# Kernel tuning notes

Hardware: AMD Instinct MI355X
Metric: run time of the kernel (lower is better)

## Reference

```python
import jax, jax.numpy as jnp
import numpy as np

EPS = 1e-5

def _graph_conv(x, src, dst, W, b, N):
    # DGL GraphConv, norm='both': D_out^{-1/2} then aggregate then D_in^{-1/2}
    ones = jnp.ones((src.shape[0],), x.dtype)
    out_deg = jnp.clip(jax.ops.segment_sum(ones, src, num_segments=N), 1.0)
    in_deg = jnp.clip(jax.ops.segment_sum(ones, dst, num_segments=N), 1.0)
    h = (x * (out_deg ** -0.5)[:, None]) @ W          # [N, out] (mult W before gather)
    agg = jax.ops.segment_sum(h[src], dst, num_segments=N)  # [N, out] irregular scatter
    return agg * (in_deg ** -0.5)[:, None] + b

def _bn_relu(h, gamma, beta):
    # BatchNorm1d in training mode: batch stats over node axis (biased var)
    mu = jnp.mean(h, axis=0)
    var = jnp.mean((h - mu) ** 2, axis=0)
    return jax.nn.relu((h - mu) * jax.lax.rsqrt(var + EPS) * gamma + beta)

def setup_inputs() -> dict:
    key = jax.random.key(0)
    ks = jax.random.split(key, 6)
    N, E, F, H, C = 100000, 1000000, 128, 128, 16
    return {
        "x": jax.random.normal(ks[0], (N, F), dtype=jnp.float32),
        "src": jax.random.randint(ks[1], (E,), 0, N, dtype=jnp.int32),
        "dst": jax.random.randint(ks[2], (E,), 0, N, dtype=jnp.int32),
        "W1": jax.random.normal(ks[3], (F, H), dtype=jnp.float32) * 0.05,
        "b1": jnp.zeros((H,), jnp.float32),
        "g1": jnp.ones((H,), jnp.float32),
        "be1": jnp.zeros((H,), jnp.float32),
        "W2": jax.random.normal(ks[4], (H, H), dtype=jnp.float32) * 0.05,
        "b2": jnp.zeros((H,), jnp.float32),
        "g2": jnp.ones((H,), jnp.float32),
        "be2": jnp.zeros((H,), jnp.float32),
        "Wc": jax.random.normal(ks[5], (H, C), dtype=jnp.float32) * 0.05,
        "bc": jnp.zeros((C,), jnp.float32),
    }

def reference(x, src, dst, W1, b1, g1, be1, W2, b2, g2, be2, Wc, bc):
    N = x.shape[0]
    h = _bn_relu(_graph_conv(x, src, dst, W1, b1, N), g1, be1)  # dropout = identity (eval)
    h = _bn_relu(_graph_conv(h, src, dst, W2, b2, N), g2, be2)
    return h @ Wc + bc  # [N, num_cls]
```

## Files before the change

### kernel.cpp

```cpp
#include <hip/hip_runtime.h>

#define FDIM 128
#define MAXDEG 64
#define GATHERB 2048
#define NREP 32

#define RSIZE 128
#define RSHIFT 7
#define RCAP 1024
#define CCAP 14336
#define PCAP 80

typedef unsigned short ushort_t;
typedef unsigned int uint_t;
typedef __attribute__((ext_vector_type(8))) short short8;
typedef __attribute__((ext_vector_type(16))) float float16;

__device__ __forceinline__ float bflo(uint_t u) { return __uint_as_float(u << 16); }
__device__ __forceinline__ float bfhi(uint_t u) { return __uint_as_float(u & 0xffff0000u); }
__device__ __forceinline__ ushort_t f2bf(float f) {
    uint_t u = __float_as_uint(f);
    return (ushort_t)((u + 0x7fffu + ((u >> 16) & 1u)) >> 16);
}
__device__ __forceinline__ uint_t pack2bf(float lo, float hi) {
    return (uint_t)f2bf(lo) | ((uint_t)f2bf(hi) << 16);
}

__global__ __launch_bounds__(256) void gemm1_kernel(
    const float* __restrict__ x, const float* __restrict__ W,
    ushort_t* __restrict__ outb, int N) {
    int idx = blockIdx.x;
    int t = threadIdx.x;
    __shared__ float xt[16][FDIM];
    int base = idx * 16;
    const float4* x4 = (const float4*)x;
#pragma unroll
    for (int i = 0; i < 2; i++) {
        int ii = t + i * 256;
        int row = ii >> 5, c4 = ii & 31;
        int grow = base + row;
        float4 v = make_float4(0.f, 0.f, 0.f, 0.f);
        if (grow < N) v = x4[(size_t)grow * 32 + c4];
        *(float4*)&xt[row][c4 * 4] = v;
    }
    __syncthreads();
    int rg = t >> 6, c = t & 63;
    float acc[4][2] = {};
    const float* Wc0 = W + c;
    for (int k4 = 0; k4 < 32; k4++) {
        float xv[16];
#pragma unroll
        for (int r = 0; r < 4; r++) {
            float4 tmp = *(const float4*)&xt[rg * 4 + r][k4 * 4];
            xv[r * 4 + 0] = tmp.x; xv[r * 4 + 1] = tmp.y;
            xv[r * 4 + 2] = tmp.z; xv[r * 4 + 3] = tmp.w;
        }
#pragma unroll
        for (int kk = 0; kk < 4; kk++) {
            float w0 = Wc0[(k4 * 4 + kk) * FDIM];
            float w1 = Wc0[(k4 * 4 + kk) * FDIM + 64];
#pragma unroll
            for (int r = 0; r < 4; r++) {
                acc[r][0] = fmaf(xv[r * 4 + kk], w0, acc[r][0]);
                acc[r][1] = fmaf(xv[r * 4 + kk], w1, acc[r][1]);
            }
        }
    }
#pragma unroll
    for (int r = 0; r < 4; r++) {
        int grow = base + rg * 4 + r;
        if (grow < N) {
            outb[(size_t)grow * FDIM + c] = f2bf(acc[r][0]);
            outb[(size_t)grow * FDIM + c + 64] = f2bf(acc[r][1]);
        }
    }
}

__global__ __launch_bounds__(256) void bucket_kernel(
    const int* __restrict__ src, const int* __restrict__ dst,
    uint_t* __restrict__ bktD, int* __restrict__ baseD,
    uint_t* __restrict__ bktS, int* __restrict__ baseS,
    int E, int P, int R) {
    __shared__ uint4 buf4[CCAP / 4];
    __shared__ int hist[RCAP];
    __shared__ int scanbuf[256];
    uint_t* buf = (uint_t*)buf4;
    int t = threadIdx.x;
    int role = blockIdx.x >= P;
    int p = role ? blockIdx.x - P : blockIdx.x;
    const int* key = role ? src : dst;
    int e0 = p * CCAP;
    int e1 = min(E, e0 + CCAP);
    int cnt = e1 - e0;

    for (int r = t; r < R; r += 256) hist[r] = 0;
    __syncthreads();
    for (int i = e0 + t; i < e1; i += 256) atomicAdd(&hist[key[i] >> RSHIFT], 1);
    __syncthreads();

    int b0 = t * 4;
    int hv[4];
    int s0 = 0;
#pragma unroll
    for (int k = 0; k < 4; k++) {
        hv[k] = (b0 + k < R) ? hist[b0 + k] : 0;
        s0 += hv[k];
    }
    scanbuf[t] = s0;
    __syncthreads();
    for (int off = 1; off < 256; off <<= 1) {
        int v = (t >= off) ? scanbuf[t - off] : 0;
        __syncthreads();
        scanbuf[t] += v;
        __syncthreads();
    }
    int run = scanbuf[t] - s0;
    int* baseG = role ? baseS : baseD;
#pragma unroll
    for (int k = 0; k < 4; k++) {
        if (b0 + k < R) {
            baseG[(b0 + k) * P + p] = run;
            hist[b0 + k] = run;
        }
        run += hv[k];
    }
    if (t == 0) baseG[R * P + p] = cnt;
    __syncthreads();

    for (int i = e0 + t; i < e1; i += 256) {
        int kv = key[i];
        int slot = atomicAdd(&hist[kv >> RSHIFT], 1);
        uint_t entry = role ? (uint_t)kv
                            : (((uint_t)(kv & (RSIZE - 1)) << 25) | (uint_t)src[i]);
        buf[slot] = entry;
    }
    __syncthreads();

    uint_t* outp = role ? bktS : bktD;
    uint4* og = (uint4*)(outp + (size_t)e0);
    int n4 = (cnt + 3) >> 2;
    for (int j = t; j < n4; j += 256) og[j] = buf4[j];
}

__global__ __launch_bounds__(256) void build_kernel(
    const uint_t* __restrict__ bktD, const int* __restrict__ baseD,
    const uint_t* __restrict__ bktS, const int* __restrict__ baseS,
    int* __restrict__ eidx, int* __restrict__ cnt, int* __restrict__ cs,
    int N, int P) {
    __shared__ uint4 ell4[RSIZE][MAXDEG / 4];
    __shared__ int cntN[RSIZE], csN[RSIZE];
    __shared__ int dB0[PCAP], dB1[PCAP], sB0[PCAP], sB1[PCAP];
    uint_t* ell = (uint_t*)ell4;
    int t = threadIdx.x;
    int r = blockIdx.x;

    if (t < RSIZE) { cntN[t] = 0; csN[t] = 0; }
    for (int i = t; i < P; i += 256) {
        dB0[i] = baseD[r * P + i];
        dB1[i] = baseD[(r + 1) * P + i];
        sB0[i] = baseS[r * P + i];
        sB1[i] = baseS[(r + 1) * P + i];
    }
    __syncthreads();

    int wave = t >> 6, lane = t & 63;
    for (int p = wave; p < P; p += 4) {
        int b = dB0[p], len = dB1[p] - b;
        const uint_t* seg = bktD + (size_t)p * CCAP + b;
        for (int i = lane; i < len; i += 64) {
            uint_t e = seg[i];
            int dl = e >> 25;
            uint_t s = e & 0x1FFFFFFu;
            int slot = atomicAdd(&cntN[dl], 1);
            if (slot < MAXDEG) ell[dl * MAXDEG + slot] = s;
        }
        int b2 = sB0[p], len2 = sB1[p] - b2;
        const uint_t* seg2 = bktS + (size_t)p * CCAP + b2;
        for (int i = lane; i < len2; i += 64)
            atomicAdd(&csN[seg2[i] & (RSIZE - 1)], 1);
    }
    __syncthreads();

    int base = r * RSIZE;
    for (int i = t; i < RSIZE * (MAXDEG / 4); i += 256) {
        int n = i >> 4, q = i & 15;
        int g = base + n;
        if (g < N && q * 4 < min(cntN[n], MAXDEG))
            ((uint4*)eidx)[(size_t)g * (MAXDEG / 4) + q] = ell4[n][q];
    }
    if (t < RSIZE) {
        int g = base + t;
        if (g < N) { cnt[g] = cntN[t]; cs[g] = csN[t]; }
    }
}

template <bool OS>
__global__ __launch_bounds__(256) void gather_kernel(const ushort_t* __restrict__ hb,
                                                     const int* __restrict__ eidx,
                                                     const int* __restrict__ cnt,
                                                     const int* __restrict__ cs,
                                                     const float* __restrict__ b,
                                                     ushort_t* __restrict__ outb,
                                                     float* __restrict__ statsRep, int N) {
    __shared__ float4 redS[256];
    __shared__ float4 redQ[256];
    int t = threadIdx.x;
    int wave = t >> 6, lane = t & 63;
    int half = lane >> 5, sub = lane & 31;
    int gw = blockIdx.x * 4 + wave;
    const uint2* h2 = (const uint2*)hb;
    uint2* o2 = (uint2*)outb;
    float4 bb = ((const float4*)b)[sub];
    float st0 = 0, st1 = 0, st2 = 0, st3 = 0, sq0 = 0, sq1 = 0, sq2 = 0, sq3 = 0;

    for (int node = gw; node < N; node += GATHERB * 4) {
        int deg = cnt[node];
        int e = min(deg, MAXDEG);
        const int* row = eidx + (size_t)node * MAXDEG;
        int ridx = (lane < e) ? row[lane] : 0;
        float scv = 1.f;
        if (OS) scv = (lane < e) ? rsqrtf((float)max(cs[ridx], 1)) : 0.f;

        float a0 = 0, a1 = 0, a2 = 0, a3 = 0;
        float c0 = 0, c1 = 0, c2 = 0, c3 = 0;
        int j = 0;
        for (; j + 3 < e; j += 4) {
            int iA = __shfl(ridx, j + half);
            int iB = __shfl(ridx, j + 2 + half);
            float sA = OS ? __shfl(scv, j + half) : 1.f;
            float sB = OS ? __shfl(scv, j + 2 + half) : 1.f;
            uint2 uA = h2[(size_t)iA * 32 + sub];
            uint2 uB = h2[(size_t)iB * 32 + sub];
            a0 = fmaf(bflo(uA.x), sA, a0); a1 = fmaf(bfhi(uA.x), sA, a1);
            a2 = fmaf(bflo(uA.y), sA, a2); a3 = fmaf(bfhi(uA.y), sA, a3);
            c0 = fmaf(bflo(uB.x), sB, c0); c1 = fmaf(bfhi(uB.x), sB, c1);
            c2 = fmaf(bflo(uB.y), sB, c2); c3 = fmaf(bfhi(uB.y), sB, c3);
        }
        for (; j < e; j += 2) {
            int jj = j + half;
            bool take = jj < e;
            int i0 = __shfl(ridx, take ? jj : (e - 1));
            float s0 = take ? (OS ? __shfl(scv, jj) : 1.f) : 0.f;
            uint2 u = h2[(size_t)i0 * 32 + sub];
            a0 = fmaf(bflo(u.x), s0, a0); a1 = fmaf(bfhi(u.x), s0, a1);
            a2 = fmaf(bflo(u.y), s0, a2); a3 = fmaf(bfhi(u.y), s0, a3);
        }
        a0 += c0; a1 += c1; a2 += c2; a3 += c3;
        a0 += __shfl_xor(a0, 32);
        a1 += __shfl_xor(a1, 32);
        a2 += __shfl_xor(a2, 32);
        a3 += __shfl_xor(a3, 32);
        if (half == 0) {
            float isc = rsqrtf((float)max(deg, 1));
            uint2 o;
            o.x = pack2bf(fmaf(a0, isc, bb.x), fmaf(a1, isc, bb.y));
            o.y = pack2bf(fmaf(a2, isc, bb.z), fmaf(a3, isc, bb.w));
            o2[(size_t)node * 32 + sub] = o;
            float v0 = bflo(o.x), v1 = bfhi(o.x), v2 = bflo(o.y), v3 = bfhi(o.y);
            st0 += v0; st1 += v1; st2 += v2; st3 += v3;
            sq0 = fmaf(v0, v0, sq0); sq1 = fmaf(v1, v1, sq1);
            sq2 = fmaf(v2, v2, sq2); sq3 = fmaf(v3, v3, sq3);
        }
    }

    redS[t] = make_float4(st0, st1, st2, st3);
    redQ[t] = make_float4(sq0, sq1, sq2, sq3);
    __syncthreads();
    if (t < 32) {
        float4 s = make_float4(0, 0, 0, 0), q = make_float4(0, 0, 0, 0);
#pragma unroll
        for (int w = 0; w < 4; w++) {
            float4 a = redS[w * 64 + t];
            float4 z = redQ[w * 64 + t];
            s.x += a.x; s.y += a.y; s.z += a.z; s.w += a.w;
            q.x += z.x; q.y += z.y; q.z += z.z; q.w += z.w;
        }
        float* dstp = statsRep + (size_t)(blockIdx.x & (NREP - 1)) * 256;
        atomicAdd(&dstp[t * 4 + 0], s.x);
        atomicAdd(&dstp[t * 4 + 1], s.y);
        atomicAdd(&dstp[t * 4 + 2], s.z);
        atomicAdd(&dstp[t * 4 + 3], s.w);
        atomicAdd(&dstp[128 + t * 4 + 0], q.x);
        atomicAdd(&dstp[128 + t * 4 + 1], q.y);
        atomicAdd(&dstp[128 + t * 4 + 2], q.z);
        atomicAdd(&dstp[128 + t * 4 + 3], q.w);
    }
}

__global__ __launch_bounds__(256) void gemm2_kernel(const ushort_t* __restrict__ hb,
                                                    const float* __restrict__ W,
                                                    const int* __restrict__ cs,
                                                    const float* __restrict__ statsRep,
                                                    const float* __restrict__ g,
                                                    const float* __restrict__ be,
                                                    ushort_t* __restrict__ outb, int N,
                                                    float invN) {
    __shared__ ushort_t zt[64][136];
    __shared__ ushort_t wt[128][136];
    __shared__ float Ash[FDIM], Bsh[FDIM];
    int t = threadIdx.x;
    int base = blockIdx.x * 64;

    if (t < FDIM) {
        float s = 0.f, q = 0.f;
        for (int r = 0; r < NREP; r++) {
            s += statsRep[r * 256 + t];
            q += statsRep[r * 256 + 128 + t];
        }
        float mu = s * invN;
        float var = q * invN - mu * mu;
        float a = g[t] * rsqrtf(var + 1e-5f);
        Ash[t] = a;
        Bsh[t] = be[t] - mu * a;
    }
    for (int i = t; i < FDIM * FDIM; i += 256) {
        int k = i >> 7, n = i & 127;
        wt[n][k] = f2bf(W[i]);
    }
    __syncthreads();

    const uint_t* h1 = (const uint_t*)hb;
    for (int i = t; i < 64 * 64; i += 256) {
        int row = i >> 6, cp = i & 63;
        int grow = base + row;
        uint_t o = 0;
        if (grow < N) {
            uint_t u = h1[(size_t)grow * 64 + cp];
            float s = rsqrtf((float)max(cs[grow], 1));
            float v0 = fmaxf(fmaf(bflo(u), Ash[cp * 2], Bsh[cp * 2]), 0.f) * s;
            float v1 = fmaxf(fmaf(bfhi(u), Ash[cp * 2 + 1], Bsh[cp * 2 + 1]), 0.f) * s;
            o = pack2bf(v0, v1);
        }
        *(uint_t*)&zt[row][cp * 2] = o;
    }
    __syncthreads();

    int wv = t >> 6, lane = t & 63;
    int rt = wv >> 1;
    int m = lane & 31;
    int kg = lane >> 5;

    short8 af[8];
#pragma unroll
    for (int kk = 0; kk < 8; kk++)
        af[kk] = *(const short8*)&zt[rt * 32 + m][kk * 16 + kg * 8];

#pragma unroll
    for (int cc = 0; cc < 2; cc++) {
        int ct = (wv & 1) * 2 + cc;
        float16 acc = {0, 0, 0, 0, 0, 0, 0, 0, 0, 0, 0, 0, 0, 0, 0, 0};
#pragma unroll
        for (int kk = 0; kk < 8; kk++) {
            short8 bf = *(const short8*)&wt[ct * 32 + m][kk * 16 + kg * 8];
            acc = __builtin_amdgcn_mfma_f32_32x32x16_bf16(af[kk], bf, acc, 0, 0, 0);
        }
        int col = ct * 32 + m;
#pragma unroll
        for (int r = 0; r < 16; r++) {
            int row = base + rt * 32 + (r & 3) + 8 * (r >> 2) + 4 * kg;
            if (row < N) outb[(size_t)row * FDIM + col] = f2bf(acc[r]);
        }
    }
}

__global__ __launch_bounds__(256) void cls_kernel(const ushort_t* __restrict__ hb,
                                                  const float* __restrict__ Wc,
                                                  const float* __restrict__ bc,
                                                  const float* __restrict__ statsRep,
                                                  const float* __restrict__ g,
                                                  const float* __restrict__ be,
                                                  float* __restrict__ out, int N, float invN) {
    __shared__ float wcl[FDIM * 16];
    __shared__ float red[16][256];
    __shared__ float Ash[FDIM], Bsh[FDIM];
    int t = threadIdx.x;
    int base = blockIdx.x * 64;
#pragma unroll
    for (int i = 0; i < 8; i++) wcl[t + i * 256] = Wc[t + i * 256];
    if (t < FDIM) {
        float s = 0.f, q = 0.f;
        for (int r = 0; r < NREP; r++) {
            s += statsRep[r * 256 + t];
            q += statsRep[r * 256 + 128 + t];
        }
        float mu = s * invN;
        float var = q * invN - mu * mu;
        float a = g[t] * rsqrtf(var + 1e-5f);
        Ash[t] = a;
        Bsh[t] = be[t] - mu * a;
    }
    __syncthreads();

    int node = base + (t >> 2);
    int q4 = t & 3;
    float acc[16];
#pragma unroll
    for (int c = 0; c < 16; c++) acc[c] = 0.f;

    if (node < N) {
        const uint2* hu2 = (const uint2*)((const uint_t*)hb + (size_t)node * 64 + q4 * 16);
        const float* Af = Ash + q4 * 32;
        const float* Bf = Bsh + q4 * 32;
#pragma unroll 1
        for (int kk = 0; kk < 8; kk++) {
            uint2 u = hu2[kk];
            float4 ab = *(const float4*)&Af[kk * 4];
            float4 bb = *(const float4*)&Bf[kk * 4];
            float v0 = fmaxf(fmaf(bflo(u.x), ab.x, bb.x), 0.f);
            float v1 = fmaxf(fmaf(bfhi(u.x), ab.y, bb.y), 0.f);
            float v2 = fmaxf(fmaf(bflo(u.y), ab.z, bb.z), 0.f);
            float v3 = fmaxf(fmaf(bfhi(u.y), ab.w, bb.w), 0.f);
            int k0 = q4 * 32 + kk * 4;
            const float* w0 = &wcl[k0 * 16];
#pragma unroll
            for (int c = 0; c < 16; c++) {
                float s = fmaf(v0, w0[c], fmaf(v1, w0[16 + c], fmaf(v2, w0[32 + c], v3 * w0[48 + c])));
                acc[c] += s;
            }
        }
    }
#pragma unroll
    for (int c = 0; c < 16; c++) red[c][t] = acc[c];
    __syncthreads();
#pragma unroll
    for (int i = t; i < 64 * 16; i += 256) {
        int n = i >> 4, c = i & 15;
        float4 p = *(const float4*)&red[c][n * 4];
        int grow = base + n;
        if (grow < N) out[(size_t)grow * 16 + c] = (p.x + p.y) + (p.z + p.w) + bc[c];
    }
}

extern "C" void kernel_launch(void* const* d_in, const int* in_sizes, int n_in,
                              void* d_out, int out_size, void* d_ws, size_t ws_size,
                              hipStream_t stream) {
    const float* x  = (const float*)d_in[0];
    const int* src  = (const int*)d_in[1];
    const int* dst  = (const int*)d_in[2];
    const float* W1 = (const float*)d_in[3];
    const float* b1 = (const float*)d_in[4];
    const float* g1 = (const float*)d_in[5];
    const float* be1= (const float*)d_in[6];
    const float* W2 = (const float*)d_in[7];
    const float* b2 = (const float*)d_in[8];
    const float* g2 = (const float*)d_in[9];
    const float* be2= (const float*)d_in[10];
    const float* Wc = (const float*)d_in[11];
    const float* bc = (const float*)d_in[12];
    float* out = (float*)d_out;

    int N = in_sizes[0] / FDIM;
    int E = in_sizes[1];
    size_t NB = (size_t)N * FDIM;

    ushort_t* bufA = (ushort_t*)d_ws;
    ushort_t* bufB = bufA + NB;
    int* cs        = (int*)(bufB + NB);
    int* cnt       = cs + N;
    float* statsR1 = (float*)(cnt + N);
    float* statsR2 = statsR1 + NREP * 256;
    int* eidx      = (int*)(statsR2 + NREP * 256);

    uint_t* bktD = (uint_t*)bufB;
    uint_t* bktS = bktD + (size_t)PCAP * CCAP;
    int* baseD   = (int*)(bktS + (size_t)PCAP * CCAP);
    int* baseS   = baseD + (RCAP + 1) * PCAP;

    int P = (E + CCAP - 1) / CCAP;
    int R = (N + RSIZE - 1) >> RSHIFT;

    hipMemsetAsync(statsR1, 0, (size_t)2 * NREP * 256 * sizeof(float), stream);

    bucket_kernel<<<2 * P, 256, 0, stream>>>(src, dst, bktD, baseD, bktS, baseS, E, P, R);
    build_kernel<<<R, 256, 0, stream>>>(bktD, baseD, bktS, baseS, eidx, cnt, cs, N, P);

    int gemmB = (N + 15) / 16;
    gemm1_kernel<<<gemmB, 256, 0, stream>>>(x, W1, bufA, N);

    float invN = 1.0f / N;

    gather_kernel<true><<<GATHERB, 256, 0, stream>>>(bufA, eidx, cnt, cs, b1, bufB, statsR1, N);

    gemm2_kernel<<<(N + 63) / 64, 256, 0, stream>>>(bufB, W2, cs, statsR1, g1, be1, bufA, N, invN);
    gather_kernel<false><<<GATHERB, 256, 0, stream>>>(bufA, eidx, cnt, nullptr, b2, bufB, statsR2, N);

    cls_kernel<<<(N + 63) / 64, 256, 0, stream>>>(bufB, Wc, bc, statsR2, g2, be2, out, N, invN);
}
```

Baseline: 390.1 us.

## Use bf16 MFMA for first GEMM and pre-convert weights once in bucket kernel

The scalar fp32 FMA gemm1 is replaced by a 64-row-tile kernel that converts x to bf16 in shared memory and computes with 32x32x16 bf16 MFMA instructions. Both weight matrices are now transposed and converted to bf16 once by extra blocks appended to the bucket kernel, so gemm1 and gemm2 load pre-packed bf16 weights with vector loads instead of converting per block. Rounding x to bf16 before the multiply lowers input precision for the first layer.

```diff
diff --git a/kernel.cpp b/kernel.cpp
--- a/kernel.cpp
+++ b/kernel.cpp
@@ -10,6 +10,7 @@
 #define RCAP 1024
 #define CCAP 14336
 #define PCAP 80
+#define WCONVB 8
 
 typedef unsigned short ushort_t;
 typedef unsigned int uint_t;
@@ -27,51 +28,56 @@
 }
 
 __global__ __launch_bounds__(256) void gemm1_kernel(
-    const float* __restrict__ x, const float* __restrict__ W,
+    const float* __restrict__ x, const ushort_t* __restrict__ wb,
     ushort_t* __restrict__ outb, int N) {
-    int idx = blockIdx.x;
+    __shared__ ushort_t zt[64][136];
+    __shared__ ushort_t wt[128][136];
     int t = threadIdx.x;
-    __shared__ float xt[16][FDIM];
-    int base = idx * 16;
+    int base = blockIdx.x * 64;
+
+    const uint4* wb4 = (const uint4*)wb;
+    for (int i = t; i < FDIM * 16; i += 256) {
+        int n = i >> 4, q = i & 15;
+        *(uint4*)&wt[n][q * 8] = wb4[n * 16 + q];
+    }
     const float4* x4 = (const float4*)x;
-#pragma unroll
-    for (int i = 0; i < 2; i++) {
-        int ii = t + i * 256;
-        int row = ii >> 5, c4 = ii & 31;
+    for (int i = t; i < 64 * 32; i += 256) {
+        int row = i >> 5, c4 = i & 31;
         int grow = base + row;
-        float4 v = make_float4(0.f, 0.f, 0.f, 0.f);
-        if (grow < N) v = x4[(size_t)grow * 32 + c4];
-        *(float4*)&xt[row][c4 * 4] = v;
-    }
-    __syncthreads();
-    int rg = t >> 6, c = t & 63;
-    float acc[4][2] = {};
-    const float* Wc0 = W + c;
-    for (int k4 = 0; k4 < 32; k4++) {
-        float xv[16];
-#pragma unroll
-        for (int r = 0; r < 4; r++) {
-            float4 tmp = *(const float4*)&xt[rg * 4 + r][k4 * 4];
-            xv[r * 4 + 0] = tmp.x; xv[r * 4 + 1] = tmp.y;
-            xv[r * 4 + 2] = tmp.z; xv[r * 4 + 3] = tmp.w;
-        }
-#pragma unroll
-        for (int kk = 0; kk < 4; kk++) {
-            float w0 = Wc0[(k4 * 4 + kk) * FDIM];
-            float w1 = Wc0[(k4 * 4 + kk) * FDIM + 64];
-#pragma unroll
-            for (int r = 0; r < 4; r++) {
-                acc[r][0] = fmaf(xv[r * 4 + kk], w0, acc[r][0]);
-                acc[r][1] = fmaf(xv[r * 4 + kk], w1, acc[r][1]);
-            }
-        }
-    }
-#pragma unroll
-    for (int r = 0; r < 4; r++) {
-        int grow = base + rg * 4 + r;
+        uint2 o = make_uint2(0u, 0u);
         if (grow < N) {
-            outb[(size_t)grow * FDIM + c] = f2bf(acc[r][0]);
-            outb[(size_t)grow * FDIM + c + 64] = f2bf(acc[r][1]);
+            float4 v = x4[(size_t)grow * 32 + c4];
+            o.x = pack2bf(v.x, v.y);
+            o.y = pack2bf(v.z, v.w);
+        }
+        *(uint2*)&zt[row][c4 * 4] = o;
+    }
+    __syncthreads();
+
+    int wv = t >> 6, lane = t & 63;
+    int rt = wv >> 1;
+    int m = lane & 31;
+    int kg = lane >> 5;
+
+    short8 af[8];
+#pragma unroll
+    for (int kk = 0; kk < 8; kk++)
+        af[kk] = *(const short8*)&zt[rt * 32 + m][kk * 16 + kg * 8];
+
+#pragma unroll
+    for (int cc = 0; cc < 2; cc++) {
+        int ct = (wv & 1) * 2 + cc;
+        float16 acc = {0, 0, 0, 0, 0, 0, 0, 0, 0, 0, 0, 0, 0, 0, 0, 0};
+#pragma unroll
+        for (int kk = 0; kk < 8; kk++) {
+            short8 bf = *(const short8*)&wt[ct * 32 + m][kk * 16 + kg * 8];
+            acc = __builtin_amdgcn_mfma_f32_32x32x16_bf16(af[kk], bf, acc, 0, 0, 0);
+        }
+        int col = ct * 32 + m;
+#pragma unroll
+        for (int r = 0; r < 16; r++) {
+            int row = base + rt * 32 + (r & 3) + 8 * (r >> 2) + 4 * kg;
+            if (row < N) outb[(size_t)row * FDIM + col] = f2bf(acc[r]);
         }
     }
 }
@@ -80,12 +86,25 @@
     const int* __restrict__ src, const int* __restrict__ dst,
     uint_t* __restrict__ bktD, int* __restrict__ baseD,
     uint_t* __restrict__ bktS, int* __restrict__ baseS,
+    const float* __restrict__ W1, const float* __restrict__ W2,
+    ushort_t* __restrict__ wb1, ushort_t* __restrict__ wb2,
     int E, int P, int R) {
     __shared__ uint4 buf4[CCAP / 4];
     __shared__ int hist[RCAP];
     __shared__ int scanbuf[256];
     uint_t* buf = (uint_t*)buf4;
     int t = threadIdx.x;
+
+    if (blockIdx.x >= 2 * P) {
+        int t0 = (blockIdx.x - 2 * P) * 256 + t;
+        for (int i = t0; i < FDIM * FDIM; i += WCONVB * 256) {
+            int k = i >> 7, n = i & 127;
+            wb1[n * FDIM + k] = f2bf(W1[i]);
+            wb2[n * FDIM + k] = f2bf(W2[i]);
+        }
+        return;
+    }
+
     int role = blockIdx.x >= P;
     int p = role ? blockIdx.x - P : blockIdx.x;
     const int* key = role ? src : dst;
@@ -288,7 +307,7 @@
 }
 
 __global__ __launch_bounds__(256) void gemm2_kernel(const ushort_t* __restrict__ hb,
-                                                    const float* __restrict__ W,
+                                                    const ushort_t* __restrict__ wb,
                                                     const int* __restrict__ cs,
                                                     const float* __restrict__ statsRep,
                                                     const float* __restrict__ g,
@@ -313,9 +332,10 @@
         Ash[t] = a;
         Bsh[t] = be[t] - mu * a;
     }
-    for (int i = t; i < FDIM * FDIM; i += 256) {
-        int k = i >> 7, n = i & 127;
-        wt[n][k] = f2bf(W[i]);
+    const uint4* wb4 = (const uint4*)wb;
+    for (int i = t; i < FDIM * 16; i += 256) {
+        int n = i >> 4, q = i & 15;
+        *(uint4*)&wt[n][q * 8] = wb4[n * 16 + q];
     }
     __syncthreads();
 
@@ -460,6 +480,8 @@
     float* statsR1 = (float*)(cnt + N);
     float* statsR2 = statsR1 + NREP * 256;
     int* eidx      = (int*)(statsR2 + NREP * 256);
+    ushort_t* wb1  = (ushort_t*)(eidx + (size_t)N * MAXDEG);
+    ushort_t* wb2  = wb1 + FDIM * FDIM;
 
     uint_t* bktD = (uint_t*)bufB;
     uint_t* bktS = bktD + (size_t)PCAP * CCAP;
@@ -471,17 +493,17 @@
 
     hipMemsetAsync(statsR1, 0, (size_t)2 * NREP * 256 * sizeof(float), stream);
 
-    bucket_kernel<<<2 * P, 256, 0, stream>>>(src, dst, bktD, baseD, bktS, baseS, E, P, R);
+    bucket_kernel<<<2 * P + WCONVB, 256, 0, stream>>>(
+        src, dst, bktD, baseD, bktS, baseS, W1, W2, wb1, wb2, E, P, R);
     build_kernel<<<R, 256, 0, stream>>>(bktD, baseD, bktS, baseS, eidx, cnt, cs, N, P);
 
-    int gemmB = (N + 15) / 16;
-    gemm1_kernel<<<gemmB, 256, 0, stream>>>(x, W1, bufA, N);
+    gemm1_kernel<<<(N + 63) / 64, 256, 0, stream>>>(x, wb1, bufA, N);
 
     float invN = 1.0f / N;
 
     gather_kernel<true><<<GATHERB, 256, 0, stream>>>(bufA, eidx, cnt, cs, b1, bufB, statsR1, N);
 
-    gemm2_kernel<<<(N + 63) / 64, 256, 0, stream>>>(bufB, W2, cs, statsR1, g1, be1, bufA, N, invN);
+    gemm2_kernel<<<(N + 63) / 64, 256, 0, stream>>>(bufB, wb2, cs, statsR1, g1, be1, bufA, N, invN);
     gather_kernel<false><<<GATHERB, 256, 0, stream>>>(bufA, eidx, cnt, nullptr, b2, bufB, statsR2, N);
 
     cls_kernel<<<(N + 63) / 64, 256, 0, stream>>>(bufB, Wc, bc, statsR2, g2, be2, out, N, invN);
```

Result: faster. 347.2 us (-11.0%).
